# Kernel tuning notes

Hardware: AMD Instinct MI355X
Metric: run time of the kernel (lower is better)

Reference implementation:

```python
import jax, jax.numpy as jnp
import numpy as np

NUM_EMBEDDINGS = 1024
EMBEDDING_DIM = 256
COMMITMENT_COST = 0.25


def setup_inputs() -> dict:
    key = jax.random.key(0)
    k1, k2 = jax.random.split(key)
    x = jax.random.normal(k1, (32, 256, 32, 32), dtype=jnp.float32)
    # torch init: uniform(-1/K, 1/K)
    lim = 1.0 / NUM_EMBEDDINGS
    codebook = jax.random.uniform(k2, (NUM_EMBEDDINGS, EMBEDDING_DIM), dtype=jnp.float32,
                                  minval=-lim, maxval=lim)
    return {"x": x, "codebook": codebook}


def reference(x, codebook):
    B, C, H, W = x.shape
    K = codebook.shape[0]
    inputs = jnp.transpose(x, (0, 2, 3, 1))          # [B,H,W,C]
    flat = inputs.reshape(-1, C)                     # [N,C]
    N = flat.shape[0]

    # squared euclidean distance via matmul expansion
    distances = (jnp.sum(flat * flat, axis=1, keepdims=True)
                 + jnp.sum(codebook * codebook, axis=1)
                 - 2.0 * flat @ codebook.T)          # [N,K]
    idx = jnp.argmin(distances, axis=1)              # [N]

    # gather lookup (same math as one-hot @ codebook)
    quantized = codebook[idx].reshape(inputs.shape)  # [B,H,W,C]

    sg = jax.lax.stop_gradient
    e_latent_loss = jnp.mean((sg(quantized) - inputs) ** 2)
    q_latent_loss = jnp.mean((quantized - sg(inputs)) ** 2)
    loss = q_latent_loss + COMMITMENT_COST * e_latent_loss

    quantized_st = inputs + sg(quantized - inputs)   # straight-through

    # avg one-hot probs via bincount-style scatter-add
    counts = jnp.zeros((K,), dtype=jnp.float32).at[idx].add(1.0)
    avg_probs = counts / N
    perplexity = jnp.exp(-jnp.sum(avg_probs * jnp.log(avg_probs + 1e-10)))

    q_out = jnp.transpose(quantized_st, (0, 3, 1, 2))  # back to NCHW
    return loss, q_out, perplexity, idx.reshape(B, H, W)
```

## Files before the change

### kernel.cpp

```cpp
#include <hip/hip_runtime.h>
#include <math.h>

#define K_    1024
#define N_    32768
#define NELEM 8388608

#define Q_OFF    1
#define PERP_OFF 8388609
#define IDX_OFF  8388610

#define XLO_F_OFF 4

typedef unsigned long long ull;
typedef _Float16 h8  __attribute__((ext_vector_type(8)));
typedef float    f4v __attribute__((ext_vector_type(4)));

#define WS_COUNTS  0
#define WS_SUMSQ   4096
#define WS_RISKCNT 4104
#define WS_DONE    4108
#define WS_EN2     4160
#define WS_XN2     8256
#define WS_IDX     139328
#define WS_RLIST   270400
#define WS_RKEY    401472
#define WS_EHI     663616
#define WS_XHI     1187904

#define ES_LD 133

#define RISKY_Q 207u


__device__ __forceinline__ unsigned u32min(unsigned a, unsigned b) { return a < b ? a : b; }
__device__ __forceinline__ unsigned u32max(unsigned a, unsigned b) { return a > b ? a : b; }

__device__ __forceinline__ void vmem_drain() {
    asm volatile("s_waitcnt vmcnt(0)" ::: "memory");
}

__global__ __launch_bounds__(256) void k_pre(const float* __restrict__ x,
                                             const float* __restrict__ cb,
                                             ushort* __restrict__ xfh,
                                             ushort* __restrict__ xfl,
                                             float* __restrict__ xn2,
                                             ushort* __restrict__ efh,
                                             float* __restrict__ en2,
                                             ull* __restrict__ rkey,
                                             unsigned* __restrict__ counts,
                                             unsigned* __restrict__ rcnt,
                                             unsigned* __restrict__ done,
                                             double* __restrict__ sumsq) {
    __shared__ float T[256 * 68];
    __shared__ double red[256];
    const int t = threadIdx.x, bid = blockIdx.x;

    if (bid < 512) {
        const int b = bid >> 4, hw0 = (bid & 15) << 6;
        const float* xb = x + b * 262144 + hw0;
#pragma unroll
        for (int i = 0; i < 16; ++i) {
            const int jv = i * 256 + t, c = jv >> 4, p4 = (jv & 15) << 2;
            const int sw = ((c >> 3) & 3) << 3;
            *(float4*)(&T[c * 68 + (p4 ^ sw)]) = *(const float4*)(xb + c * 1024 + p4);
        }
        __syncthreads();
        const int mi = t >> 6, lane = t & 63;
        const int quad = (t >> 4) & 3, l15 = t & 15;
        const int pxs = (mi * 16 + l15) ^ (quad << 3);
        double sn = 0.0;
        const size_t obase = (size_t)bid * 16384 + lane * 8;
#pragma unroll
        for (int dc = 0; dc < 8; ++dc) {
            union { _Float16 h[8]; int4 v; } ph, pl;
#pragma unroll
            for (int j = 0; j < 8; ++j) {
                const float v = T[(dc * 32 + quad * 8 + j) * 68 + pxs];
                sn += (double)v * v;
                const _Float16 hi = (_Float16)v;
                ph.h[j] = hi;
                pl.h[j] = (_Float16)((v - (float)hi) * 2048.0f);
            }
            *(int4*)(xfh + obase + (dc * 4 + mi) * 512) = ph.v;
            *(int4*)(xfl + obase + (dc * 4 + mi) * 512) = pl.v;
        }
        red[t] = sn;
        __syncthreads();
        if (t < 64) {
            const int base = (t >> 4) * 64 + (t & 15);
            xn2[bid * 64 + t] = (float)(red[base] + red[base + 16] +
                                        red[base + 32] + red[base + 48]);
        }
    } else if (bid < 528) {
        const int n = (bid - 512) * 64 + (t >> 2);
        const int seg = t & 3;
        const float* src = cb + (size_t)n * 256 + seg * 64;
        const int kt = n >> 8, wch = (n >> 6) & 3, ci = (n >> 4) & 3, l15 = n & 15;
        double s = 0.0;
#pragma unroll
        for (int g = 0; g < 8; ++g) {
            const float4 a = *(const float4*)(src + g * 8);
            const float4 b = *(const float4*)(src + g * 8 + 4);
            s += (double)a.x * a.x + (double)a.y * a.y + (double)a.z * a.z + (double)a.w * a.w;
            s += (double)b.x * b.x + (double)b.y * b.y + (double)b.z * b.z + (double)b.w * b.w;
            const float v[8] = {a.x, a.y, a.z, a.w, b.x, b.y, b.z, b.w};
            union { _Float16 h[8]; int4 q; } ph;
#pragma unroll
            for (int j = 0; j < 8; ++j)
                ph.h[j] = (_Float16)(v[j] * 1024.0f);
            const int dc = seg * 2 + (g >> 2);
            const int quad = g & 3;
            const size_t addr = ((size_t)(((kt * 4 + wch) * 8 + dc) * 4 + ci) * 64 +
                                 (quad * 16 + l15)) * 8;
            *(int4*)(efh + addr) = ph.q;
        }
        red[t] = s;
        __syncthreads();
        if (t < 64) {
            const int r2 = (bid - 512) * 64 + t;
            en2[r2] = (float)(red[t * 4] + red[t * 4 + 1] + red[t * 4 + 2] + red[t * 4 + 3]);
        }
    } else {
        const int ib = bid - 528;
        const int i0 = ib * 512 + t * 2;
        rkey[i0] = ~0ull; rkey[i0 + 1] = ~0ull;
        if (ib == 0) {
            ((uint4*)counts)[t] = make_uint4(0u, 0u, 0u, 0u);
            if (t == 0) { *rcnt = 0u; *done = 0u; *sumsq = 0.0; }
        }
    }
}

__global__ __launch_bounds__(256, 2) void k_sweep(const float* __restrict__ x,
                                                  ushort* __restrict__ xfh,
                                                  ushort* __restrict__ xfl,
                                                  const ushort* __restrict__ efh,
                                                  const float* __restrict__ en2,
                                                  int* __restrict__ idxv,
                                                  int* __restrict__ rlist,
                                                  unsigned* __restrict__ rcnt) {
    __shared__ __align__(16) ushort Bsh[16384];
    __shared__ __align__(16) ushort Bsl[16384];
    __shared__ __align__(16) float  enS[1024];
    __shared__ unsigned Mg[4][64][2];
    __shared__ int rpixS[64];
    __shared__ int rnS;

    const int t = threadIdx.x, bid = blockIdx.x;
    const int p0 = bid << 6;
    const int w = t >> 6, lane = t & 63;
    const int quad = lane >> 4, l15 = lane & 15;

    {
        const size_t base = (size_t)bid * 16384;
#pragma unroll
        for (int i = 0; i < 8; ++i) {
            const int off = (i * 256 + t) * 8;
            *(int4*)(&Bsh[off]) = *(const int4*)(xfh + base + off);
            *(int4*)(&Bsl[off]) = *(const int4*)(xfl + base + off);
        }
#pragma unroll
        for (int i = 0; i < 4; ++i)
            enS[i * 256 + t] = fmaf(en2[i * 256 + t], 1048576.0f, 131072.0f);
    }
    __syncthreads();

    unsigned K1[4], K2[4];
#pragma unroll
    for (int ni = 0; ni < 4; ++ni) { K1[ni] = 0xFFFFFFFFu; K2[ni] = 0xFFFFFFFFu; }

    for (int kt = 0; kt < 4; ++kt) {
        const f4v z = {0.f, 0.f, 0.f, 0.f};
        f4v acc1[4][4], acc2[4][4];
#pragma unroll
        for (int mi = 0; mi < 4; ++mi)
#pragma unroll
            for (int ni = 0; ni < 4; ++ni) { acc1[mi][ni] = z; acc2[mi][ni] = z; }

#pragma unroll 2
        for (int dc = 0; dc < 8; ++dc) {
            h8 ah[4];
            const size_t abase = ((size_t)((kt * 4 + w) * 8 + dc) * 4) * 512 + lane * 8;
#pragma unroll
            for (int mi = 0; mi < 4; ++mi)
                ah[mi] = *(const h8*)(efh + abase + mi * 512);
            const int bbase = dc * 2048 + lane * 8;
#pragma unroll
            for (int ni = 0; ni < 4; ++ni) {
                const h8 bh = *(const h8*)(&Bsh[bbase + ni * 512]);
                const h8 bl = *(const h8*)(&Bsl[bbase + ni * 512]);
#pragma unroll
                for (int mi = 0; mi < 4; ++mi) {
                    acc1[mi][ni] = __builtin_amdgcn_mfma_f32_16x16x32_f16(
                        ah[mi], bh, acc1[mi][ni], 0, 0, 0);
                    acc2[mi][ni] = __builtin_amdgcn_mfma_f32_16x16x32_f16(
                        ah[mi], bl, acc2[mi][ni], 0, 0, 0);
                }
            }
        }
#pragma unroll
        for (int mi = 0; mi < 4; ++mi) {
            const int cbase = kt * 256 + w * 64 + mi * 16 + quad * 4;
            const f4v enQ = *(const f4v*)(&enS[cbase]);
#pragma unroll
            for (int ni = 0; ni < 4; ++ni) {
#pragma unroll
                for (int r = 0; r < 4; ++r) {
                    const float t0 = fmaf(-2048.0f, acc1[mi][ni][r], enQ[r]);
                    const float qf = t0 - acc2[mi][ni][r];
                    const unsigned key = ((unsigned)(int)qf << 10) | (unsigned)(cbase + r);
                    const unsigned o1 = K1[ni];
                    K1[ni] = u32min(o1, key);
                    K2[ni] = u32min(K2[ni], u32max(o1, key));
                }
            }
        }
    }
#pragma unroll
    for (int m = 16; m <= 32; m <<= 1) {
#pragma unroll
        for (int ni = 0; ni < 4; ++ni) {
            const unsigned a1 = (unsigned)__shfl_xor((int)K1[ni], m, 64);
            const unsigned a2 = (unsigned)__shfl_xor((int)K2[ni], m, 64);
            const unsigned n1 = u32min(K1[ni], a1);
            const unsigned n2 = u32min(u32max(K1[ni], a1), u32min(K2[ni], a2));
            K1[ni] = n1; K2[ni] = n2;
        }
    }
    if (quad == 0) {
#pragma unroll
        for (int ni = 0; ni < 4; ++ni) {
            Mg[w][ni * 16 + l15][0] = K1[ni];
            Mg[w][ni * 16 + l15][1] = K2[ni];
        }
    }
    __syncthreads();
    if (t < 64) {
        unsigned b1 = Mg[0][t][0], b2 = Mg[0][t][1];
#pragma unroll
        for (int ww = 1; ww < 4; ++ww) {
            const unsigned a1 = Mg[ww][t][0], a2 = Mg[ww][t][1];
            const unsigned n1 = u32min(b1, a1);
            b2 = u32min(u32max(b1, a1), u32min(b2, a2));
            b1 = n1;
        }
        const int P = p0 + t;
        idxv[P] = (int)(b1 & 1023u);
        const bool risky = ((b2 >> 10) - (b1 >> 10)) <= RISKY_Q;
        const ull mask = __ballot(risky);
        const int pre = __popcll(mask & ((1ull << t) - 1ull));
        unsigned base = 0;
        if (t == 0) { base = atomicAdd(rcnt, (unsigned)__popcll(mask)); rnS = (int)__popcll(mask); }
        base = (unsigned)__shfl((int)base, 0, 64);
        if (risky) { rlist[base + pre] = P; rpixS[pre] = t; }
    }
    __syncthreads();
    {
        const int rn = rnS;
        float* xth = (float*)(xfh + (size_t)bid * 16384);
        float* xtl = (float*)(xfl + (size_t)bid * 16384);
        for (int i = w; i < rn; i += 4) {
            const int lp = rpixS[i];
            const int P = p0 + lp;
            const float* xp = x + (size_t)(P >> 10) * 262144 + (P & 1023);
            const int c0 = lane * 4;
            float4 vv;
            vv.x = xp[(size_t)(c0 + 0) * 1024];
            vv.y = xp[(size_t)(c0 + 1) * 1024];
            vv.z = xp[(size_t)(c0 + 2) * 1024];
            vv.w = xp[(size_t)(c0 + 3) * 1024];
            float* dst = (c0 < 128) ? (xth + lp * 128 + c0)
                                    : (xtl + lp * 128 + (c0 - 128));
            *(float4*)dst = vv;
        }
    }
}

__global__ __launch_bounds__(256) void k_rescan(const float* __restrict__ xth,
                                                const float* __restrict__ xtl,
                                                const float* __restrict__ cb,
                                                const float* __restrict__ en2,
                                                const float* __restrict__ xn2,
                                                const int* __restrict__ rlist,
                                                const unsigned* __restrict__ rcnt,
                                                ull* __restrict__ rkey) {
    __shared__ float xs[64 * 68];
    __shared__ float es[64 * ES_LD];
    __shared__ int plist[64];
    const int t = threadIdx.x;
    const unsigned cnt = *rcnt;
    const int nunits = (int)(((cnt + 63) >> 6) << 3);
    const int ti = t >> 4, tj = t & 15;

    for (int u = blockIdx.x; u < nunits; u += gridDim.x) {
        const int tile = u >> 3, kt = u & 7;
        __syncthreads();
        if (t < 64) {
            const int li = tile * 64 + t;
            plist[t] = rlist[li < (int)cnt ? li : 0];
        }
        __syncthreads();

        float xnr[4]; int pid[4];
#pragma unroll
        for (int r = 0; r < 4; ++r) {
            pid[r] = plist[ti * 4 + r];
            xnr[r] = xn2[pid[r]];
        }
        float acc[4][8];
#pragma unroll
        for (int r = 0; r < 4; ++r)
#pragma unroll
            for (int j = 0; j < 8; ++j) acc[r][j] = 0.f;
        float best_s[4]; int best_k[4];
#pragma unroll
        for (int r = 0; r < 4; ++r) { best_s[r] = INFINITY; best_k[r] = 0; }

        for (int dc = 0; dc < 4; ++dc) {
            __syncthreads();
            {
                const int p = t & 63, coff = t >> 6;
                const int P = plist[p];
                const size_t rbase = (size_t)(P >> 6) * 8192 + (size_t)(P & 63) * 128;
                const int c0 = dc * 64 + coff * 16;
                const float* src = (c0 < 128) ? (xth + rbase + c0)
                                              : (xtl + rbase + (c0 - 128));
#pragma unroll
                for (int q = 0; q < 4; ++q) {
                    const float4 v = *(const float4*)(src + q * 4);
                    const int cl = coff * 16 + q * 4;
                    xs[(cl + 0) * 68 + p] = v.x;
                    xs[(cl + 1) * 68 + p] = v.y;
                    xs[(cl + 2) * 68 + p] = v.z;
                    xs[(cl + 3) * 68 + p] = v.w;
                }
            }
#pragma unroll
            for (int i = 0; i < 8; ++i) {
                const int jv = i * 256 + t, k = jv >> 4, d4 = (jv & 15) << 2;
                const float4 v = *(const float4*)(cb + (size_t)(kt * 128 + k) * 256 + dc * 64 + d4);
                es[(d4 + 0) * ES_LD + k] = v.x; es[(d4 + 1) * ES_LD + k] = v.y;
                es[(d4 + 2) * ES_LD + k] = v.z; es[(d4 + 3) * ES_LD + k] = v.w;
            }
            __syncthreads();
#pragma unroll 4
            for (int d = 0; d < 64; ++d) {
                const float4 xv = *(const float4*)(&xs[d * 68 + ti * 4]);
                const float4 e0 = *(const float4*)(&es[d * ES_LD + tj * 8]);
                const float4 e1 = *(const float4*)(&es[d * ES_LD + tj * 8 + 4]);
                const float xr[4] = {xv.x, xv.y, xv.z, xv.w};
                const float ej[8] = {e0.x, e0.y, e0.z, e0.w, e1.x, e1.y, e1.z, e1.w};
#pragma unroll
                for (int r = 0; r < 4; ++r)
#pragma unroll
                    for (int j = 0; j < 8; ++j)
                        acc[r][j] = fmaf(xr[r], ej[j], acc[r][j]);
            }
        }
#pragma unroll
        for (int j = 0; j < 8; ++j) {
            const int k = kt * 128 + tj * 8 + j;
            const float en = en2[k];
#pragma unroll
            for (int r = 0; r < 4; ++r) {
                const float s1 = xnr[r] + en;
                const float dist = fmaf(-2.f, acc[r][j], s1);
                if (dist < best_s[r] || (dist == best_s[r] && k < best_k[r])) {
                    best_s[r] = dist; best_k[r] = k;
                }
            }
        }
#pragma unroll
        for (int r = 0; r < 4; ++r) {
            float s = best_s[r]; int k = best_k[r];
            for (int m = 1; m < 16; m <<= 1) {
                const float s2 = __shfl_xor(s, m, 64);
                const int k2 = __shfl_xor(k, m, 64);
                if (s2 < s || (s2 == s && k2 < k)) { s = s2; k = k2; }
            }
            if (tj == 0 && (tile * 64 + ti * 4 + r) < (int)cnt) {
                const ull key = ((ull)__float_as_uint(s) << 32) | (unsigned)k;
                atomicMin(&rkey[pid[r]], key);
            }
        }
    }
}

__global__ __launch_bounds__(256) void k_gather(const float* __restrict__ x,
                                                const float* __restrict__ cb,
                                                const int* __restrict__ idxv,
                                                const ull* __restrict__ rkey,
                                                float* __restrict__ out,
                                                double* __restrict__ psum,
                                                unsigned* __restrict__ counts,
                                                unsigned* __restrict__ done) {
    __shared__ __align__(16) float cs[32 * 260];
    __shared__ int   kidx[32];
    __shared__ float wpart[4];
    __shared__ int   lastf;
    __shared__ double part[256];
    __shared__ double part2[256];

    const int t = threadIdx.x, bid = blockIdx.x;
    const int n0 = bid * 32;
    if (t < 32) {
        const int n = n0 + t;
        const ull rk = rkey[n];
        const int kk = (rk != ~0ull) ? (int)(unsigned)(rk & 0xffffffffu) : idxv[n];
        kidx[t] = kk;
        atomicAdd(&counts[kk], 1u);
        out[IDX_OFF + n] = (float)kk;
    }
    if (t == 0) lastf = 0;
    __syncthreads();
#pragma unroll
    for (int i = 0; i < 8; ++i) {
        int jv = (i << 8) + t;
        int p = jv >> 6, c4 = (jv & 63) << 2;
        const float4 v = *(const float4*)(cb + (size_t)kidx[p] * 256 + c4);
        *(float4*)(&cs[p * 260 + c4]) = v;
    }
    __syncthreads();

    const int b = bid >> 5, h = bid & 31;
    const float* xb = x + b * 262144 + h * 32;
    float* qb = out + Q_OFF + b * 262144 + h * 32;

    float local = 0.f;
#pragma unroll
    for (int i = 0; i < 8; ++i) {
        int j = (i << 8) + t;
        int c = j >> 3, w4 = (j & 7) << 2;
        const float q0 = cs[(w4 + 0) * 260 + c];
        const float q1 = cs[(w4 + 1) * 260 + c];
        const float q2 = cs[(w4 + 2) * 260 + c];
        const float q3 = cs[(w4 + 3) * 260 + c];
        const float4 xv = *(const float4*)(xb + c * 1024 + w4);
        const float d0 = q0 - xv.x, d1 = q1 - xv.y;
        const float d2 = q2 - xv.z, d3 = q3 - xv.w;
        local += d0 * d0 + d1 * d1 + d2 * d2 + d3 * d3;
        qb[c * 1024 + w4 + 0] = q0;
        qb[c * 1024 + w4 + 1] = q1;
        qb[c * 1024 + w4 + 2] = q2;
        qb[c * 1024 + w4 + 3] = q3;
    }
    for (int m = 32; m > 0; m >>= 1) local += __shfl_down(local, m, 64);
    if ((t & 63) == 0) wpart[t >> 6] = local;
    __syncthreads();
    if (t == 0) {
        const double bs = (double)wpart[0] + (double)wpart[1] +
                          (double)wpart[2] + (double)wpart[3];
        atomicExch((ull*)&psum[bid], (ull)__double_as_longlong(bs));
        vmem_drain();
        if (atomicAdd(done, 1u) == 1023u) lastf = 1;
    }
    __syncthreads();
    if (lastf) {
        double s = 0.0, ss = 0.0;
        for (int k = t; k < K_; k += 256) {
            const unsigned c = atomicAdd(&counts[k], 0u);
            const double p = (double)c / (double)N_;
            s += p * log(p + 1e-10);
        }
#pragma unroll
        for (int i = 0; i < 4; ++i) {
            const ull pv = atomicAdd((ull*)&psum[i * 256 + t], 0ull);
            ss += __longlong_as_double((long long)pv);
        }
        part[t] = s; part2[t] = ss;
        __syncthreads();
        for (int off = 128; off > 0; off >>= 1) {
            if (t < off) { part[t] += part[t + off]; part2[t] += part2[t + off]; }
            __syncthreads();
        }
        if (t == 0) {
            out[PERP_OFF] = (float)exp(-part[0]);
            out[0] = (float)(part2[0] * 1.25 / (double)NELEM);
        }
    }
}

extern "C" void kernel_launch(void* const* d_in, const int* in_sizes, int n_in,
                              void* d_out, int out_size, void* d_ws, size_t ws_size,
                              hipStream_t stream) {
    const float* x  = (const float*)d_in[0];
    const float* cb = (const float*)d_in[1];
    float* out = (float*)d_out;
    char*  ws  = (char*)d_ws;

    unsigned* counts = (unsigned*)(ws + WS_COUNTS);
    double*   sumsq  = (double*)(ws + WS_SUMSQ);
    unsigned* rcnt   = (unsigned*)(ws + WS_RISKCNT);
    unsigned* done   = (unsigned*)(ws + WS_DONE);
    float*    en2    = (float*)(ws + WS_EN2);
    float*    xn2    = (float*)(ws + WS_XN2);
    int*      idxv   = (int*)(ws + WS_IDX);
    int*      rlist  = (int*)(ws + WS_RLIST);
    ull*      rkey   = (ull*)(ws + WS_RKEY);
    ushort*   efh    = (ushort*)(ws + WS_EHI);
    ushort*   xfh    = (ushort*)(ws + WS_XHI);
    ushort*   xfl    = (ushort*)(out + XLO_F_OFF);
    double*   psum   = (double*)(ws + WS_RLIST);

    k_pre<<<592, 256, 0, stream>>>(x, cb, xfh, xfl, xn2, efh, en2,
                                   rkey, counts, rcnt, done, sumsq);
    k_sweep<<<512, 256, 0, stream>>>(x, xfh, xfl, efh, en2, idxv, rlist, rcnt);
    k_rescan<<<512, 256, 0, stream>>>((const float*)xfh, (const float*)xfl,
                                      cb, en2, xn2, rlist, rcnt, rkey);
    k_gather<<<1024, 256, 0, stream>>>(x, cb, idxv, rkey, out, psum, counts, done);
}
```

Measured before the change: 189.7 us.

## Fuse input transpose and fp16 hi/lo split into sweep kernel prologue

The per-pixel transpose, fp16 hi/lo split and squared-norm computation of x move out of the preprocessing kernel and into the start of the sweep kernel. The split values are written straight into shared memory instead of round-tripping through global buffers. The preprocessing kernel shrinks to codebook preparation and workspace zeroing. In exchange, the sweep prologue now loops over eight channel chunks with two barriers each, and uses more shared memory.

Result: faster. 184.5 us, median of 2 (-2.7%).

```diff
diff --git a/kernel.cpp b/kernel.cpp
--- a/kernel.cpp
+++ b/kernel.cpp
@@ -39,60 +39,19 @@
     asm volatile("s_waitcnt vmcnt(0)" ::: "memory");
 }
 
-__global__ __launch_bounds__(256) void k_pre(const float* __restrict__ x,
-                                             const float* __restrict__ cb,
-                                             ushort* __restrict__ xfh,
-                                             ushort* __restrict__ xfl,
-                                             float* __restrict__ xn2,
-                                             ushort* __restrict__ efh,
-                                             float* __restrict__ en2,
-                                             ull* __restrict__ rkey,
-                                             unsigned* __restrict__ counts,
-                                             unsigned* __restrict__ rcnt,
-                                             unsigned* __restrict__ done,
-                                             double* __restrict__ sumsq) {
-    __shared__ float T[256 * 68];
+__global__ __launch_bounds__(256) void k_pre0(const float* __restrict__ cb,
+                                              ushort* __restrict__ efh,
+                                              float* __restrict__ en2,
+                                              ull* __restrict__ rkey,
+                                              unsigned* __restrict__ counts,
+                                              unsigned* __restrict__ rcnt,
+                                              unsigned* __restrict__ done,
+                                              double* __restrict__ sumsq) {
     __shared__ double red[256];
     const int t = threadIdx.x, bid = blockIdx.x;
 
-    if (bid < 512) {
-        const int b = bid >> 4, hw0 = (bid & 15) << 6;
-        const float* xb = x + b * 262144 + hw0;
-#pragma unroll
-        for (int i = 0; i < 16; ++i) {
-            const int jv = i * 256 + t, c = jv >> 4, p4 = (jv & 15) << 2;
-            const int sw = ((c >> 3) & 3) << 3;
-            *(float4*)(&T[c * 68 + (p4 ^ sw)]) = *(const float4*)(xb + c * 1024 + p4);
-        }
-        __syncthreads();
-        const int mi = t >> 6, lane = t & 63;
-        const int quad = (t >> 4) & 3, l15 = t & 15;
-        const int pxs = (mi * 16 + l15) ^ (quad << 3);
-        double sn = 0.0;
-        const size_t obase = (size_t)bid * 16384 + lane * 8;
-#pragma unroll
-        for (int dc = 0; dc < 8; ++dc) {
-            union { _Float16 h[8]; int4 v; } ph, pl;
-#pragma unroll
-            for (int j = 0; j < 8; ++j) {
-                const float v = T[(dc * 32 + quad * 8 + j) * 68 + pxs];
-                sn += (double)v * v;
-                const _Float16 hi = (_Float16)v;
-                ph.h[j] = hi;
-                pl.h[j] = (_Float16)((v - (float)hi) * 2048.0f);
-            }
-            *(int4*)(xfh + obase + (dc * 4 + mi) * 512) = ph.v;
-            *(int4*)(xfl + obase + (dc * 4 + mi) * 512) = pl.v;
-        }
-        red[t] = sn;
-        __syncthreads();
-        if (t < 64) {
-            const int base = (t >> 4) * 64 + (t & 15);
-            xn2[bid * 64 + t] = (float)(red[base] + red[base + 16] +
-                                        red[base + 32] + red[base + 48]);
-        }
-    } else if (bid < 528) {
-        const int n = (bid - 512) * 64 + (t >> 2);
+    if (bid < 16) {
+        const int n = bid * 64 + (t >> 2);
         const int seg = t & 3;
         const float* src = cb + (size_t)n * 256 + seg * 64;
         const int kt = n >> 8, wch = (n >> 6) & 3, ci = (n >> 4) & 3, l15 = n & 15;
@@ -117,11 +76,11 @@
         red[t] = s;
         __syncthreads();
         if (t < 64) {
-            const int r2 = (bid - 512) * 64 + t;
+            const int r2 = bid * 64 + t;
             en2[r2] = (float)(red[t * 4] + red[t * 4 + 1] + red[t * 4 + 2] + red[t * 4 + 3]);
         }
     } else {
-        const int ib = bid - 528;
+        const int ib = bid - 16;
         const int i0 = ib * 512 + t * 2;
         rkey[i0] = ~0ull; rkey[i0 + 1] = ~0ull;
         if (ib == 0) {
@@ -136,13 +95,15 @@
                                                   ushort* __restrict__ xfl,
                                                   const ushort* __restrict__ efh,
                                                   const float* __restrict__ en2,
+                                                  float* __restrict__ xn2,
                                                   int* __restrict__ idxv,
                                                   int* __restrict__ rlist,
                                                   unsigned* __restrict__ rcnt) {
     __shared__ __align__(16) ushort Bsh[16384];
     __shared__ __align__(16) ushort Bsl[16384];
     __shared__ __align__(16) float  enS[1024];
-    __shared__ unsigned Mg[4][64][2];
+    __shared__ __align__(16) float  T8[32 * 68];
+    __shared__ union { unsigned mg[4][64][2]; double red[256]; } U;
     __shared__ int rpixS[64];
     __shared__ int rnS;
 
@@ -152,18 +113,45 @@
     const int quad = lane >> 4, l15 = lane & 15;
 
     {
-        const size_t base = (size_t)bid * 16384;
-#pragma unroll
-        for (int i = 0; i < 8; ++i) {
-            const int off = (i * 256 + t) * 8;
-            *(int4*)(&Bsh[off]) = *(const int4*)(xfh + base + off);
-            *(int4*)(&Bsl[off]) = *(const int4*)(xfl + base + off);
+        const int b = bid >> 4, hw0 = (bid & 15) << 6;
+        const float* xb = x + b * 262144 + hw0;
+        const int quad_p = (t >> 4) & 3;
+        const int pxs = (w * 16 + l15) ^ (quad_p << 3);
+        double sn = 0.0;
+        for (int dc = 0; dc < 8; ++dc) {
+#pragma unroll
+            for (int i = 0; i < 2; ++i) {
+                const int jv = i * 256 + t, lc = jv >> 4, p4 = (jv & 15) << 2;
+                const int sw = ((lc >> 3) & 3) << 3;
+                *(float4*)(&T8[lc * 68 + (p4 ^ sw)]) =
+                    *(const float4*)(xb + (dc * 32 + lc) * 1024 + p4);
+            }
+            __syncthreads();
+            union { _Float16 h[8]; int4 v; } ph, pl;
+#pragma unroll
+            for (int j = 0; j < 8; ++j) {
+                const float v = T8[(quad_p * 8 + j) * 68 + pxs];
+                sn += (double)v * v;
+                const _Float16 hi = (_Float16)v;
+                ph.h[j] = hi;
+                pl.h[j] = (_Float16)((v - (float)hi) * 2048.0f);
+            }
+            *(int4*)(&Bsh[(dc * 4 + w) * 512 + lane * 8]) = ph.v;
+            *(int4*)(&Bsl[(dc * 4 + w) * 512 + lane * 8]) = pl.v;
+            __syncthreads();
+        }
+        U.red[t] = sn;
+        __syncthreads();
+        if (t < 64) {
+            const int base = (t >> 4) * 64 + (t & 15);
+            xn2[bid * 64 + t] = (float)(U.red[base] + U.red[base + 16] +
+                                        U.red[base + 32] + U.red[base + 48]);
         }
 #pragma unroll
         for (int i = 0; i < 4; ++i)
             enS[i * 256 + t] = fmaf(en2[i * 256 + t], 1048576.0f, 131072.0f);
-    }
-    __syncthreads();
+        __syncthreads();
+    }
 
     unsigned K1[4], K2[4];
 #pragma unroll
@@ -230,16 +218,16 @@
     if (quad == 0) {
 #pragma unroll
         for (int ni = 0; ni < 4; ++ni) {
-            Mg[w][ni * 16 + l15][0] = K1[ni];
-            Mg[w][ni * 16 + l15][1] = K2[ni];
+            U.mg[w][ni * 16 + l15][0] = K1[ni];
+            U.mg[w][ni * 16 + l15][1] = K2[ni];
         }
     }
     __syncthreads();
     if (t < 64) {
-        unsigned b1 = Mg[0][t][0], b2 = Mg[0][t][1];
+        unsigned b1 = U.mg[0][t][0], b2 = U.mg[0][t][1];
 #pragma unroll
         for (int ww = 1; ww < 4; ++ww) {
-            const unsigned a1 = Mg[ww][t][0], a2 = Mg[ww][t][1];
+            const unsigned a1 = U.mg[ww][t][0], a2 = U.mg[ww][t][1];
             const unsigned n1 = u32min(b1, a1);
             b2 = u32min(u32max(b1, a1), u32min(b2, a2));
             b1 = n1;
@@ -502,9 +490,8 @@
     ushort*   xfl    = (ushort*)(out + XLO_F_OFF);
     double*   psum   = (double*)(ws + WS_RLIST);
 
-    k_pre<<<592, 256, 0, stream>>>(x, cb, xfh, xfl, xn2, efh, en2,
-                                   rkey, counts, rcnt, done, sumsq);
-    k_sweep<<<512, 256, 0, stream>>>(x, xfh, xfl, efh, en2, idxv, rlist, rcnt);
+    k_pre0<<<80, 256, 0, stream>>>(cb, efh, en2, rkey, counts, rcnt, done, sumsq);
+    k_sweep<<<512, 256, 0, stream>>>(x, xfh, xfl, efh, en2, xn2, idxv, rlist, rcnt);
     k_rescan<<<512, 256, 0, stream>>>((const float*)xfh, (const float*)xfl,
                                       cb, en2, xn2, rlist, rcnt, rkey);
     k_gather<<<1024, 256, 0, stream>>>(x, cb, idxv, rkey, out, psum, counts, done);
```
